# Optimization experiments

Hardware: AMD Instinct MI355X
Metric: run time of the kernel (lower is better)

## Reference

```python
import jax, jax.numpy as jnp
import numpy as np

N_NODES = 100000
N_EDGES = 1600000
EMB_DIM = 128
BN_EPS = 1e-5


def setup_inputs() -> dict:
    key = jax.random.key(0)
    k = jax.random.split(key, 5)
    x = jax.random.normal(k[0], (N_NODES, EMB_DIM), dtype=jnp.float32)
    src = jax.random.randint(k[1], (N_EDGES,), 0, N_NODES)
    dst = jax.random.randint(k[2], (N_EDGES,), 0, N_NODES)
    W = jax.random.normal(k[3], (EMB_DIM, EMB_DIM), dtype=jnp.float32) / np.float32(np.sqrt(EMB_DIM))
    b = jnp.zeros((EMB_DIM,), dtype=jnp.float32)
    gamma = jnp.ones((EMB_DIM,), dtype=jnp.float32)
    beta = jnp.zeros((EMB_DIM,), dtype=jnp.float32)
    return {"x": x, "src": src, "dst": dst, "W": W, "b": b, "gamma": gamma, "beta": beta}


def reference(x, src, dst, W, b, gamma, beta):
    n = x.shape[0]
    ones = jnp.ones(src.shape, dtype=x.dtype)
    # DGL GraphConv norm='both': degrees clamped to min 1
    deg_out = jnp.maximum(jax.ops.segment_sum(ones, src, num_segments=n), 1.0)
    deg_in = jnp.maximum(jax.ops.segment_sum(ones, dst, num_segments=n), 1.0)
    norm_src = jax.lax.rsqrt(deg_out)  # [N]
    norm_dst = jax.lax.rsqrt(deg_in)   # [N]
    # W applied before aggregation (in_feats == out_feats path in DGL)
    h = (x * norm_src[:, None]) @ W                              # [N, D]
    agg = jax.ops.segment_sum(h[src], dst, num_segments=n)       # SpMM gather/scatter, [N, D]
    h = agg * norm_dst[:, None] + b                              # [N, D]
    # BatchNorm1d over nodes (training-mode batch stats, biased variance)
    mean = jnp.mean(h, axis=0)
    var = jnp.var(h, axis=0)
    h = (h - mean) * jax.lax.rsqrt(var + BN_EPS) * gamma + beta
    h = jax.nn.relu(h)
    # dropout: identity in eval-mode reference
    return h + x  # residual
```

## Files before the change

kernel.cpp:

```cpp
#include <hip/hip_runtime.h>
#include <hip/hip_bf16.h>

#define NN 100000
#define NE 1600000
#define D  128
#define BN_EPS 1e-5f

#define CB  782
#define NC  256
#define EPC (NE / NC)
#define NSLICE  7
#define SLICESZ 15400
#define SCH     32
#define EPH (NE / SCH)

typedef __attribute__((ext_vector_type(8))) short bf16x8;
typedef __attribute__((ext_vector_type(4))) float f32x4;

#define WLD 136

static __device__ __forceinline__ ushort f2bf(float f) {
    __hip_bfloat16 b = __float2bfloat16(f);
    return *reinterpret_cast<ushort*>(&b);
}
static __device__ __forceinline__ float bflo(unsigned v) {
    return __uint_as_float((v & 0xffffu) << 16);
}
static __device__ __forceinline__ float bfhi(unsigned v) {
    return __uint_as_float(v & 0xffff0000u);
}

__global__ void k_wcast(const float* __restrict__ W, ushort* __restrict__ WT) {
    int i = blockIdx.x * 256 + threadIdx.x;
    int n = i >> 7, k = i & 127;
    WT[i] = f2bf(W[k * D + n]);
}


__global__ __launch_bounds__(256) void k_ccount(const int* __restrict__ dst,
                                                int* __restrict__ P ) {
    __shared__ int hist[CB];
    const int c = blockIdx.x;
    const int t = threadIdx.x;
    for (int i = t; i < CB; i += 256) hist[i] = 0;
    __syncthreads();
    const int base = c * EPC;
    for (int i = t; i < EPC; i += 256)
        atomicAdd(&hist[dst[base + i] >> 7], 1);
    __syncthreads();
    for (int i = t; i < CB; i += 256) P[i * NC + c] = hist[i];
}

__global__ __launch_bounds__(256) void k_cscanA(int* __restrict__ P,
                                                int* __restrict__ bintotal) {
    __shared__ int sh[NC];
    const int b = blockIdx.x;
    const int t = threadIdx.x;
    const int v = P[b * NC + t];
    sh[t] = v;
    __syncthreads();
    for (int off = 1; off < NC; off <<= 1) {
        int u = (t >= off) ? sh[t - off] : 0;
        __syncthreads();
        sh[t] += u;
        __syncthreads();
    }
    P[b * NC + t] = sh[t] - v;
    if (t == NC - 1) bintotal[b] = sh[t];
}

__global__ __launch_bounds__(1024) void k_cscanB(const int* __restrict__ bintotal,
                                                 int* __restrict__ binbase) {
    __shared__ int sh[1024];
    const int t = threadIdx.x;
    const int v = (t < CB) ? bintotal[t] : 0;
    sh[t] = v;
    __syncthreads();
    for (int off = 1; off < 1024; off <<= 1) {
        int u = (t >= off) ? sh[t - off] : 0;
        __syncthreads();
        sh[t] += u;
        __syncthreads();
    }
    if (t < CB) binbase[t] = sh[t] - v;
    if (t == CB - 1) binbase[CB] = sh[t];
}

__global__ __launch_bounds__(256) void k_cscatter(const int* __restrict__ dst,
                                                  const int* __restrict__ src,
                                                  const int* __restrict__ P,
                                                  const int* __restrict__ binbase,
                                                  int* __restrict__ sedge) {
    __shared__ int cur[CB];
    const int c = blockIdx.x;
    const int t = threadIdx.x;
    for (int i = t; i < CB; i += 256) cur[i] = binbase[i] + P[i * NC + c];
    __syncthreads();
    const int base = c * EPC;
    for (int i = t; i < EPC; i += 256) {
        int d = dst[base + i];
        int pos = atomicAdd(&cur[d >> 7], 1);
        sedge[pos] = src[base + i] | ((d & 127) << 17);
    }
}

__global__ __launch_bounds__(256) void k_fine(const int* __restrict__ sedge,
                                              const int* __restrict__ binbase,
                                              int* __restrict__ ptr,
                                              int* __restrict__ esrc) {
    __shared__ int fh[128], fp[128], fcur[128];
    const int b = blockIdx.x;
    const int t = threadIdx.x;
    const int lo = binbase[b], hi = binbase[b + 1];
    if (t < 128) fh[t] = 0;
    __syncthreads();
    for (int i = lo + t; i < hi; i += 256)
        atomicAdd(&fh[(unsigned)sedge[i] >> 17], 1);
    __syncthreads();
    if (t < 128) fp[t] = fh[t];
    __syncthreads();
    for (int off = 1; off < 128; off <<= 1) {
        int u = (t < 128 && t >= off) ? fp[t - off] : 0;
        __syncthreads();
        if (t < 128) fp[t] += u;
        __syncthreads();
    }
    if (t < 128) {
        const int node = b * 128 + t;
        const int ex = fp[t] - fh[t];
        fcur[t] = ex;
        if (node < NN) {
            ptr[node] = lo + ex;
        } else if (node == NN) {
            ptr[NN] = lo + ex;
        }
    }
    __syncthreads();
    for (int i = lo + t; i < hi; i += 256) {
        unsigned v = (unsigned)sedge[i];
        int pos = atomicAdd(&fcur[v >> 17], 1);
        esrc[lo + pos] = v & 0x1FFFF;
    }
}


__global__ __launch_bounds__(256) void k_shist(const int* __restrict__ src,
                                               int* __restrict__ SP ) {
    __shared__ int hist[SLICESZ];
    const int s = blockIdx.x / SCH;
    const int c = blockIdx.x % SCH;
    const int t = threadIdx.x;
    const int lo = s * SLICESZ;
    for (int i = t; i < SLICESZ; i += 256) hist[i] = 0;
    __syncthreads();
    const int base = c * EPH;
    for (int i = t; i < EPH; i += 256) {
        int k = src[base + i] - lo;
        if ((unsigned)k < (unsigned)SLICESZ) atomicAdd(&hist[k], 1);
    }
    __syncthreads();
    int* out = SP + ((size_t)s * SCH + c) * SLICESZ;
    for (int i = t; i < SLICESZ; i += 256) out[i] = hist[i];
}

__global__ void k_smerge(const int* __restrict__ SP, float* __restrict__ degout) {
    int n = blockIdx.x * 256 + threadIdx.x;
    if (n >= NN) return;
    const int s = n / SLICESZ, k = n % SLICESZ;
    const int* col = SP + ((size_t)s * SCH) * SLICESZ + k;
    int sum = 0;
#pragma unroll
    for (int c = 0; c < SCH; ++c) sum += col[(size_t)c * SLICESZ];
    degout[n] = (float)sum;
}

__global__ __launch_bounds__(256) void k_gemm(const float* __restrict__ x,
                                              const float* __restrict__ degout,
                                              const ushort* __restrict__ WT,
                                              ushort* __restrict__ h) {
    __shared__ ushort Wl[D * WLD];

    const int t = threadIdx.x;
    for (int s = t; s < 2048; s += 256) {
        int row = s >> 4, slot = s & 15;
        uint4 v = *reinterpret_cast<const uint4*>(WT + row * D + slot * 8);
        *reinterpret_cast<uint4*>(&Wl[row * WLD + slot * 8]) = v;
    }
    __syncthreads();

    const int wave = t >> 6;
    const int lane = t & 63;
    const int m16  = lane & 15;
    const int kq   = lane >> 4;
    const int row  = blockIdx.x * 64 + wave * 16 + m16;
    const int rc   = row < NN ? row : NN - 1;

    const float nrm = rsqrtf(fmaxf(degout[rc], 1.0f));

    bf16x8 afrag[4];
    const float* xr = x + (size_t)rc * D + kq * 8;
#pragma unroll
    for (int kt = 0; kt < 4; ++kt) {
        f32x4 lo = *reinterpret_cast<const f32x4*>(xr + kt * 32);
        f32x4 hi = *reinterpret_cast<const f32x4*>(xr + kt * 32 + 4);
        union { bf16x8 v; ushort u[8]; } af;
#pragma unroll
        for (int j = 0; j < 4; ++j) {
            af.u[j]     = f2bf(lo[j] * nrm);
            af.u[4 + j] = f2bf(hi[j] * nrm);
        }
        afrag[kt] = af.v;
    }

    f32x4 acc[8];
#pragma unroll
    for (int nt = 0; nt < 8; ++nt) acc[nt] = (f32x4)(0.0f);

#pragma unroll
    for (int kt = 0; kt < 4; ++kt) {
#pragma unroll
        for (int nt = 0; nt < 8; ++nt) {
            int n = nt * 16 + m16;
            const bf16x8 bfrag = *reinterpret_cast<const bf16x8*>(
                &Wl[n * WLD + kt * 32 + kq * 8]);
            acc[nt] = __builtin_amdgcn_mfma_f32_16x16x32_bf16(afrag[kt], bfrag, acc[nt], 0, 0, 0);
        }
    }

    const int orow = blockIdx.x * 64 + wave * 16 + kq * 4;
#pragma unroll
    for (int nt = 0; nt < 8; ++nt) {
#pragma unroll
        for (int r = 0; r < 4; ++r) {
            int rr = orow + r;
            if (rr < NN) h[(size_t)rr * D + nt * 16 + m16] = f2bf(acc[nt][r]);
        }
    }
}

__global__ __launch_bounds__(256) void k_agg(const ushort* __restrict__ h,
                                             const int* __restrict__ ptr,
                                             const int* __restrict__ esrc,
                                             const float* __restrict__ b,
                                             ushort* __restrict__ h2) {
    const int node = blockIdx.x * 4 + (threadIdx.x >> 6);
    const int lane = threadIdx.x & 63;
    if (node >= NN) return;
    const int s0 = ptr[node];
    const int s1 = ptr[node + 1];
    const int eg = lane >> 4;
    const int cb = (lane & 15) * 8;

    float acc[8];
#pragma unroll
    for (int j = 0; j < 8; ++j) acc[j] = 0.0f;

    for (int i = s0; i < s1; i += 16) {
        int  idx[4];
        bool p[4];
        uint4 v[4];
#pragma unroll
        for (int u = 0; u < 4; ++u) {
            int ii = i + eg + 4 * u;
            p[u] = ii < s1;
            if (p[u]) idx[u] = esrc[ii];
        }
#pragma unroll
        for (int u = 0; u < 4; ++u)
            if (p[u]) v[u] = *reinterpret_cast<const uint4*>(h + (size_t)idx[u] * D + cb);
#pragma unroll
        for (int u = 0; u < 4; ++u) {
            if (p[u]) {
                acc[0] += bflo(v[u].x); acc[1] += bfhi(v[u].x);
                acc[2] += bflo(v[u].y); acc[3] += bfhi(v[u].y);
                acc[4] += bflo(v[u].z); acc[5] += bfhi(v[u].z);
                acc[6] += bflo(v[u].w); acc[7] += bfhi(v[u].w);
            }
        }
    }
#pragma unroll
    for (int j = 0; j < 8; ++j) {
        acc[j] += __shfl_xor(acc[j], 16, 64);
        acc[j] += __shfl_xor(acc[j], 32, 64);
    }
    if (eg == 0) {
        const float nrm = rsqrtf(fmaxf((float)(s1 - s0), 1.0f));
        uint4 o;
        unsigned w[4];
#pragma unroll
        for (int m = 0; m < 4; ++m) {
            float e0 = acc[2 * m]     * nrm + b[cb + 2 * m];
            float e1 = acc[2 * m + 1] * nrm + b[cb + 2 * m + 1];
            w[m] = (unsigned)f2bf(e0) | ((unsigned)f2bf(e1) << 16);
        }
        o.x = w[0]; o.y = w[1]; o.z = w[2]; o.w = w[3];
        *reinterpret_cast<uint4*>(h2 + (size_t)node * D + cb) = o;
    }
}

__global__ __launch_bounds__(256) void k_stats(const unsigned* __restrict__ h2u,
                                               float* __restrict__ stats) {
    __shared__ float red[4][256];
    const int t = threadIdx.x;
    float s1lo = 0.f, s1hi = 0.f, s2lo = 0.f, s2hi = 0.f;
    const int total = NN * (D / 2);
    const int stride = gridDim.x * 256;
    for (int i = blockIdx.x * 256 + t; i < total; i += stride) {
        unsigned v = h2u[i];
        float lo = bflo(v), hi = bfhi(v);
        s1lo += lo; s1hi += hi;
        s2lo += lo * lo; s2hi += hi * hi;
    }
    red[0][t] = s1lo; red[1][t] = s1hi; red[2][t] = s2lo; red[3][t] = s2hi;
    __syncthreads();
    if (t < 64) {
        const int c = t * 2;
        float a0 = red[0][t] + red[0][t + 64] + red[0][t + 128] + red[0][t + 192];
        float a1 = red[1][t] + red[1][t + 64] + red[1][t + 128] + red[1][t + 192];
        float q0 = red[2][t] + red[2][t + 64] + red[2][t + 128] + red[2][t + 192];
        float q1 = red[3][t] + red[3][t + 64] + red[3][t + 128] + red[3][t + 192];
        atomicAdd(&stats[c], a0);
        atomicAdd(&stats[c + 1], a1);
        atomicAdd(&stats[128 + c], q0);
        atomicAdd(&stats[128 + c + 1], q1);
    }
}

__global__ void k_final(const uint2* __restrict__ h2v, const float4* __restrict__ xv,
                        const float* __restrict__ gamma, const float* __restrict__ beta,
                        const float* __restrict__ stats, float4* __restrict__ outv) {
    const int i = blockIdx.x * 256 + threadIdx.x;
    const int total = NN * (D / 4);
    if (i >= total) return;
    const int c = (i & 31) * 4;
    const float inv_n = 1.0f / (float)NN;
    uint2 v = h2v[i];
    float4 xx = xv[i];
    float hv[4] = { bflo(v.x), bfhi(v.x), bflo(v.y), bfhi(v.y) };
    float xr[4] = { xx.x, xx.y, xx.z, xx.w };
    float o[4];
#pragma unroll
    for (int m = 0; m < 4; ++m) {
        float mean = stats[c + m] * inv_n;
        float var  = stats[128 + c + m] * inv_n - mean * mean;
        float t = (hv[m] - mean) * rsqrtf(var + BN_EPS) * gamma[c + m] + beta[c + m];
        o[m] = fmaxf(t, 0.0f) + xr[m];
    }
    float4 ov; ov.x = o[0]; ov.y = o[1]; ov.z = o[2]; ov.w = o[3];
    outv[i] = ov;
}

extern "C" void kernel_launch(void* const* d_in, const int* in_sizes, int n_in,
                              void* d_out, int out_size, void* d_ws, size_t ws_size,
                              hipStream_t stream) {
    const float* x     = (const float*)d_in[0];
    const int*   src   = (const int*)d_in[1];
    const int*   dst   = (const int*)d_in[2];
    const float* W     = (const float*)d_in[3];
    const float* b     = (const float*)d_in[4];
    const float* gamma = (const float*)d_in[5];
    const float* beta  = (const float*)d_in[6];
    float* out = (float*)d_out;

    float* ws     = (float*)d_ws;
    ushort* h2    = (ushort*)ws;
    float* degout = ws + (size_t)NN * D;
    float* stats  = degout + NN;
    int*   ptr    = (int*)(stats + 256);
    int*   esrc   = ptr + (NN + 1);
    ushort* WT    = (ushort*)(esrc + NE);

    int* sedge    = (int*)ws;
    int* SP       = sedge + NE;
    int* P        = SP + (size_t)NSLICE * SCH * SLICESZ;
    int* bintotal = P + (size_t)CB * NC;
    int* binbase  = bintotal + CB;

    ushort* h = (ushort*)d_out;

    hipMemsetAsync(stats, 0, 256 * sizeof(float), stream);

    k_wcast<<<64, 256, 0, stream>>>(W, WT);
    k_ccount<<<NC, 256, 0, stream>>>(dst, P);
    k_cscanA<<<CB, 256, 0, stream>>>(P, bintotal);
    k_cscanB<<<1, 1024, 0, stream>>>(bintotal, binbase);
    k_cscatter<<<NC, 256, 0, stream>>>(dst, src, P, binbase, sedge);
    k_shist<<<NSLICE * SCH, 256, 0, stream>>>(src, SP);
    k_smerge<<<(NN + 255) / 256, 256, 0, stream>>>(SP, degout);
    k_gemm<<<(NN + 63) / 64, 256, 0, stream>>>(x, degout, WT, h);
    k_fine<<<CB, 256, 0, stream>>>(sedge, binbase, ptr, esrc);
    k_agg<<<(NN + 3) / 4, 256, 0, stream>>>(h, ptr, esrc, b, h2);
    k_stats<<<1024, 256, 0, stream>>>((const unsigned*)h2, stats);
    k_final<<<(NN * (D / 4) + 255) / 256, 256, 0, stream>>>((const uint2*)h2, (const float4*)x,
                                                            gamma, beta, stats, (float4*)out);
}
```

Measured before the change: 277.3 us.

## Pack degree histogram into 16-bit halves and split aggregation by column half

The source-degree histogram now packs two 16-bit counters per shared-memory int, so each slice covers twice as many nodes and only 4 slices are needed instead of 7. This cuts redundant passes over the src array and shrinks the partial-histogram buffer. The aggregation kernel is split into two launches, each gathering one 64-column half of every neighbour row with 8 edges in flight per wave. The split aims to halve the working set of h per pass for better cache hit rates, at the cost of reading the CSR indices twice and doubling launch count.

```diff
diff --git a/kernel.cpp b/kernel.cpp
--- a/kernel.cpp
+++ b/kernel.cpp
@@ -9,8 +9,9 @@
 #define CB  782
 #define NC  256
 #define EPC (NE / NC)
-#define NSLICE  7
-#define SLICESZ 15400
+#define NSLICE  4
+#define SLICESZ 30800
+#define SW      (SLICESZ / 2)
 #define SCH     32
 #define EPH (NE / SCH)
 
@@ -146,32 +147,40 @@
 
 __global__ __launch_bounds__(256) void k_shist(const int* __restrict__ src,
                                                int* __restrict__ SP ) {
-    __shared__ int hist[SLICESZ];
+    __shared__ int hist[SW];
     const int s = blockIdx.x / SCH;
     const int c = blockIdx.x % SCH;
     const int t = threadIdx.x;
     const int lo = s * SLICESZ;
-    for (int i = t; i < SLICESZ; i += 256) hist[i] = 0;
+    for (int i = t; i < SW; i += 256) hist[i] = 0;
     __syncthreads();
     const int base = c * EPH;
     for (int i = t; i < EPH; i += 256) {
         int k = src[base + i] - lo;
-        if ((unsigned)k < (unsigned)SLICESZ) atomicAdd(&hist[k], 1);
-    }
-    __syncthreads();
-    int* out = SP + ((size_t)s * SCH + c) * SLICESZ;
-    for (int i = t; i < SLICESZ; i += 256) out[i] = hist[i];
+        if ((unsigned)k < (unsigned)SLICESZ)
+            atomicAdd(&hist[k >> 1], 1 << ((k & 1) * 16));
+    }
+    __syncthreads();
+    int* out = SP + ((size_t)s * SCH + c) * SW;
+    for (int i = t; i < SW; i += 256) out[i] = hist[i];
 }
 
 __global__ void k_smerge(const int* __restrict__ SP, float* __restrict__ degout) {
-    int n = blockIdx.x * 256 + threadIdx.x;
-    if (n >= NN) return;
-    const int s = n / SLICESZ, k = n % SLICESZ;
-    const int* col = SP + ((size_t)s * SCH) * SLICESZ + k;
-    int sum = 0;
-#pragma unroll
-    for (int c = 0; c < SCH; ++c) sum += col[(size_t)c * SLICESZ];
-    degout[n] = (float)sum;
+    int w = blockIdx.x * 256 + threadIdx.x;
+    if (w >= (NN + 1) / 2) return;
+    const int n = w * 2;
+    const int s = n / SLICESZ;
+    const int k = n - s * SLICESZ;
+    const int* col = SP + ((size_t)s * SCH) * SW + (k >> 1);
+    int lo = 0, hi = 0;
+#pragma unroll
+    for (int c = 0; c < SCH; ++c) {
+        int v = col[(size_t)c * SW];
+        lo += v & 0xFFFF;
+        hi += (v >> 16) & 0xFFFF;
+    }
+    degout[n] = (float)lo;
+    if (n + 1 < NN) degout[n + 1] = (float)hi;
 }
 
 __global__ __launch_bounds__(256) void k_gemm(const float* __restrict__ x,
@@ -238,6 +247,7 @@
     }
 }
 
+template<int HALF>
 __global__ __launch_bounds__(256) void k_agg(const ushort* __restrict__ h,
                                              const int* __restrict__ ptr,
                                              const int* __restrict__ esrc,
@@ -248,28 +258,28 @@
     if (node >= NN) return;
     const int s0 = ptr[node];
     const int s1 = ptr[node + 1];
-    const int eg = lane >> 4;
-    const int cb = (lane & 15) * 8;
+    const int eg = lane >> 3;
+    const int cb = HALF * 64 + (lane & 7) * 8;
 
     float acc[8];
 #pragma unroll
     for (int j = 0; j < 8; ++j) acc[j] = 0.0f;
 
     for (int i = s0; i < s1; i += 16) {
-        int  idx[4];
-        bool p[4];
-        uint4 v[4];
-#pragma unroll
-        for (int u = 0; u < 4; ++u) {
-            int ii = i + eg + 4 * u;
+        int  idx[2];
+        bool p[2];
+        uint4 v[2];
+#pragma unroll
+        for (int u = 0; u < 2; ++u) {
+            int ii = i + eg + 8 * u;
             p[u] = ii < s1;
             if (p[u]) idx[u] = esrc[ii];
         }
 #pragma unroll
-        for (int u = 0; u < 4; ++u)
+        for (int u = 0; u < 2; ++u)
             if (p[u]) v[u] = *reinterpret_cast<const uint4*>(h + (size_t)idx[u] * D + cb);
 #pragma unroll
-        for (int u = 0; u < 4; ++u) {
+        for (int u = 0; u < 2; ++u) {
             if (p[u]) {
                 acc[0] += bflo(v[u].x); acc[1] += bfhi(v[u].x);
                 acc[2] += bflo(v[u].y); acc[3] += bfhi(v[u].y);
@@ -280,6 +290,7 @@
     }
 #pragma unroll
     for (int j = 0; j < 8; ++j) {
+        acc[j] += __shfl_xor(acc[j], 8, 64);
         acc[j] += __shfl_xor(acc[j], 16, 64);
         acc[j] += __shfl_xor(acc[j], 32, 64);
     }
@@ -372,7 +383,7 @@
 
     int* sedge    = (int*)ws;
     int* SP       = sedge + NE;
-    int* P        = SP + (size_t)NSLICE * SCH * SLICESZ;
+    int* P        = SP + (size_t)NSLICE * SCH * SW;
     int* bintotal = P + (size_t)CB * NC;
     int* binbase  = bintotal + CB;
 
@@ -386,10 +397,11 @@
     k_cscanB<<<1, 1024, 0, stream>>>(bintotal, binbase);
     k_cscatter<<<NC, 256, 0, stream>>>(dst, src, P, binbase, sedge);
     k_shist<<<NSLICE * SCH, 256, 0, stream>>>(src, SP);
-    k_smerge<<<(NN + 255) / 256, 256, 0, stream>>>(SP, degout);
+    k_smerge<<<((NN + 1) / 2 + 255) / 256, 256, 0, stream>>>(SP, degout);
     k_gemm<<<(NN + 63) / 64, 256, 0, stream>>>(x, degout, WT, h);
     k_fine<<<CB, 256, 0, stream>>>(sedge, binbase, ptr, esrc);
-    k_agg<<<(NN + 3) / 4, 256, 0, stream>>>(h, ptr, esrc, b, h2);
+    k_agg<0><<<(NN + 3) / 4, 256, 0, stream>>>(h, ptr, esrc, b, h2);
+    k_agg<1><<<(NN + 3) / 4, 256, 0, stream>>>(h, ptr, esrc, b, h2);
     k_stats<<<1024, 256, 0, stream>>>((const unsigned*)h2, stats);
     k_final<<<(NN * (D / 4) + 255) / 256, 256, 0, stream>>>((const uint2*)h2, (const float4*)x,
                                                             gamma, beta, stats, (float4*)out);
```

Result: slower. 305.6 us (+10.2%).
